# Kernel optimization log

Hardware: AMD Instinct MI355X
Metric: run time of the kernel (lower is better)

The kernel has to match this reference:

```python
import jax, jax.numpy as jnp
import numpy as np
from jax import lax

B, T, V, E, H, M = 512, 60, 50000, 300, 512, 256


def _lstm_final_h(x_emb, seqlen, kernel, bias):
    """BasicLSTMCell (gate order i,j,f,o; forget_bias=1.0) with dynamic_rnn
    sequence_length semantics: state stops updating at t >= seqlen.
    x_emb: [B, T, E]; returns final h: [B, H]."""
    b = x_emb.shape[0]
    h0 = jnp.zeros((b, H), x_emb.dtype)
    c0 = jnp.zeros((b, H), x_emb.dtype)

    def step(carry, inp):
        c, h = carry
        xt, t = inp
        z = jnp.concatenate([xt, h], axis=1) @ kernel + bias  # [B, 4H]
        i, j, f, o = jnp.split(z, 4, axis=1)
        nc = c * jax.nn.sigmoid(f + 1.0) + jax.nn.sigmoid(i) * jnp.tanh(j)
        nh = jnp.tanh(nc) * jax.nn.sigmoid(o)
        valid = (t < seqlen)[:, None]
        return (jnp.where(valid, nc, c), jnp.where(valid, nh, h)), None

    (c, h), _ = lax.scan(step, (c0, h0),
                         (jnp.swapaxes(x_emb, 0, 1), jnp.arange(T)))
    return h


def setup_inputs() -> dict:
    key = jax.random.key(0)
    ks = jax.random.split(key, 8)
    return {
        "input1": jax.random.randint(ks[0], (B, T), 0, V, dtype=jnp.int32),
        "input2": jax.random.randint(ks[1], (B, T), 0, V, dtype=jnp.int32),
        "seqlen1": jax.random.randint(ks[2], (B,), 1, T + 1, dtype=jnp.int32),
        "seqlen2": jax.random.randint(ks[3], (B,), 1, T + 1, dtype=jnp.int32),
        "embeddings": jax.random.normal(ks[4], (V, E), jnp.float32) * 0.1,
        "lstm_kernel": jax.random.normal(ks[5], (E + H, 4 * H), jnp.float32) * 0.02,
        "lstm_bias": jnp.zeros((4 * H,), jnp.float32),
        "W1": jax.random.normal(ks[6], (4 * (H + 1) + 1, M), jnp.float32) * 0.02,
        "b1": jnp.zeros((1, M), jnp.float32),
        "W2": jax.random.normal(ks[7], (M, 2), jnp.float32) * 0.02,
        "b2": jnp.zeros((1, 2), jnp.float32),
    }


def reference(input1, input2, seqlen1, seqlen2, embeddings,
              lstm_kernel, lstm_bias, W1, b1, W2, b2):
    x1 = embeddings[input1]  # [B, T, E]
    x2 = embeddings[input2]
    h1 = _lstm_final_h(x1, seqlen1, lstm_kernel, lstm_bias)  # [B, H]
    h2 = _lstm_final_h(x2, seqlen2, lstm_kernel, lstm_bias)
    len1 = (seqlen1.astype(jnp.float32) / float(T))[:, None]
    len2 = (seqlen2.astype(jnp.float32) / float(T))[:, None]
    h1 = jnp.concatenate([h1, len1], axis=1)  # [B, H+1]
    h2 = jnp.concatenate([h2, len2], axis=1)
    h_sub = h1 - h2
    h_dist = jnp.sum(h_sub * h_sub, axis=1, keepdims=True)  # [B, 1]
    h_mul = h1 * h2
    h_combined = jnp.concatenate([h1, h2, h_sub, h_dist, h_mul], axis=1)
    e1 = jax.nn.relu(h_combined @ W1 + b1)  # dropout keep_prob=1 -> identity
    preds = e1 @ W2 + b2  # [B, 2]
    return preds
```

## Files before the change

kernel.cpp:

```cpp
#include <hip/hip_runtime.h>
#include <hip/hip_bf16.h>

#define BATCH 512
#define TT 60
#define EDIM 300
#define HDIM 512
#define KREAL 812
#define KP 896
#define KP1 2112
#define MDIM 256

typedef __bf16 bf16x4 __attribute__((ext_vector_type(4)));
typedef __bf16 bf16x8 __attribute__((ext_vector_type(8)));
typedef float  f32x16 __attribute__((ext_vector_type(16)));

#define GLL16(g, l) __builtin_amdgcn_global_load_lds( \
    (const __attribute__((address_space(1))) void*)(g), \
    (__attribute__((address_space(3))) void*)(l), 16, 0, 0)

__device__ __forceinline__ float sigm(float x) {
    return 1.0f / (1.0f + __expf(-x));
}
__device__ __forceinline__ float tanh_fast(float x) {
    float e = __expf(-2.0f * fabsf(x));
    float r = (1.0f - e) / (1.0f + e);
    return x >= 0.0f ? r : -r;
}


__global__ __launch_bounds__(256) void sort_rows(const int* __restrict__ sl1,
                                                 const int* __restrict__ sl2,
                                                 int* __restrict__ rowinfo,
                                                 unsigned* __restrict__ nact) {
    __shared__ unsigned cnt[61];
    __shared__ unsigned off[61];
    int tid = threadIdx.x;
    if (tid < 61) cnt[tid] = 0;
    __syncthreads();
    for (int i = tid; i < 1024; i += 256) {
        int sl = (i < 512) ? sl1[i] : sl2[i - 512];
        atomicAdd(&cnt[60 - sl], 1u);
    }
    __syncthreads();
    if (tid == 0) {
        unsigned s = 0;
        for (int k = 0; k < 61; ++k) { off[k] = s; s += cnt[k]; }
        for (int t = 0; t < 60; ++t) {
            unsigned act = off[60 - t];
            nact[t] = (act + 63) >> 6;
        }
    }
    __syncthreads();
    for (int i = tid; i < 1024; i += 256) {
        int sc = i >= 512;
        int b = i & 511;
        int sl = sc ? sl2[b] : sl1[b];
        unsigned pos = atomicAdd(&off[60 - sl], 1u);
        rowinfo[pos] = b | (sc << 15) | (sl << 20);
    }
}

__global__ __launch_bounds__(256) void prep_w(const float* __restrict__ kern,
                                              __bf16* __restrict__ wf) {
    __shared__ float tile[64][65];
    int bk = blockIdx.x % 14;
    int bn = blockIdx.x / 14;
    int k0 = bk * 64, n0 = bn * 64;
    int tid = threadIdx.x;
#pragma unroll
    for (int i = 0; i < 16; ++i) {
        int id = i * 256 + tid;
        int kk = id >> 6, nn = id & 63;
        int kg = k0 + kk;
        int src = (kg < 300) ? kg : (kg >= 384 ? kg - 84 : -1);
        tile[kk][nn] = (src >= 0) ? kern[(size_t)src * 2048 + n0 + nn] : 0.0f;
    }
    __syncthreads();
    int gate = n0 >> 9;
    int nt = gate >> 1;
#pragma unroll
    for (int i = 0; i < 2; ++i) {
        int id = i * 256 + tid;
        int nn = id >> 3, k8 = id & 7;
        bf16x8 hv, lv;
#pragma unroll
        for (int j = 0; j < 8; ++j) {
            float v = tile[k8 * 8 + j][nn];
            __bf16 h = (__bf16)v;
            hv[j] = h;
            lv[j] = (__bf16)(v - (float)h);
        }
        int cg = (((n0 & 511) >> 4) + (nn >> 4));
        int hc = nn & 15;
        int lzc = ((gate & 1) << 4) + hc;
        int kglob = k0 + k8 * 8;
        int c = kglob >> 7;
        int j = (kglob >> 4) & 7;
        int half = k8 & 1;
        size_t o = (size_t)cg * 114688 + c * 16384 + (j * 4 + nt * 2) * 512
                 + (half * 32 + lzc) * 8;
        *(bf16x8*)(wf + o) = hv;
        *(bf16x8*)(wf + o + 512) = lv;
    }
}

__global__ __launch_bounds__(256) void prep_w1(const float* __restrict__ W1,
                                               __bf16* __restrict__ w1h,
                                               __bf16* __restrict__ w1l) {
    __shared__ float tile[64][65];
    int bk = blockIdx.x % 33;
    int bn = blockIdx.x / 33;
    int k0 = bk * 64, n0 = bn * 64;
    int tid = threadIdx.x;
#pragma unroll
    for (int i = 0; i < 16; ++i) {
        int id = i * 256 + tid;
        int kk = id >> 6, nn = id & 63;
        int kg = k0 + kk;
        tile[kk][nn] = (kg < 2053) ? W1[(size_t)kg * MDIM + n0 + nn] : 0.0f;
    }
    __syncthreads();
#pragma unroll
    for (int i = 0; i < 2; ++i) {
        int id = i * 256 + tid;
        int nn = id >> 3, k8 = (id & 7) * 8;
        bf16x8 hv, lv;
#pragma unroll
        for (int j = 0; j < 8; ++j) {
            float v = tile[k8 + j][nn];
            __bf16 h = (__bf16)v;
            hv[j] = h;
            lv[j] = (__bf16)(v - (float)h);
        }
        size_t o = (size_t)(n0 + nn) * KP1 + k0 + k8;
        *(bf16x8*)(w1h + o) = hv;
        *(bf16x8*)(w1l + o) = lv;
    }
}

__device__ __forceinline__ void emb_unit(int tok, int rl, int rr, int bt,
                                         const float* __restrict__ emb,
                                         __bf16* Xfn) {
    const float* er = emb + (size_t)tok * EDIM + rr * 8;
    float4 f0 = *(const float4*)er;
    float4 f1 = (rr == 37) ? make_float4(0.f, 0.f, 0.f, 0.f)
                           : *(const float4*)(er + 4);
    float vv[8] = {f0.x, f0.y, f0.z, f0.w, f1.x, f1.y, f1.z, f1.w};
    bf16x8 hv, lv;
#pragma unroll
    for (int j = 0; j < 8; ++j) {
        __bf16 h = (__bf16)vv[j];
        hv[j] = h;
        lv[j] = (__bf16)(vv[j] - (float)h);
    }
    int ke = rr * 8;
    int c = ke >> 7, kl = ke & 127;
    int kg = kl >> 6, jj = (kl >> 4) & 3, half = (kl >> 3) & 1;
    int s = rl >> 5;
    size_t base = ((((size_t)bt * 2 + s) * 2 + kg) * 7 + c) * 4096 + jj * 1024
                + (half * 32 + (rl & 31)) * 8;
    *(bf16x8*)(Xfn + base) = hv;
    *(bf16x8*)(Xfn + base + 512) = lv;
}

__global__ __launch_bounds__(256) void prep_x0(const int* __restrict__ in1,
                                               const int* __restrict__ in2,
                                               const int* __restrict__ rowinfo,
                                               const float* __restrict__ emb,
                                               __bf16* __restrict__ Xf) {
    __shared__ int tk[64];
    int bt = blockIdx.x >> 5, cg = blockIdx.x & 31;
    int tid = threadIdx.x;
    if (tid < 64) {
        int info = rowinfo[bt * 64 + tid];
        int b = info & 511, sc = (info >> 15) & 1;
        tk[tid] = (sc ? in2 : in1)[b * TT];
    }
    __syncthreads();
    if (tid < 76) {
        int id = tid * 32 + cg;
        int rl = id / 38, rr = id - rl * 38;
        emb_unit(tk[rl], rl, rr, bt, emb, Xf);
    }
}

#define ZSTR 72

__global__ __launch_bounds__(256, 2) void lstm_step(
    int t,
    const int* __restrict__ in1, const int* __restrict__ in2,
    const int* __restrict__ rowinfo, const unsigned* __restrict__ nact,
    const float* __restrict__ emb, const float* __restrict__ bias,
    const __bf16* __restrict__ wf,
    const __bf16* __restrict__ Xf, __bf16* __restrict__ Xfn,
    float* __restrict__ h_state, float* __restrict__ c_state) {

    int bx = blockIdx.x;
    int bt = bx >> 5;
    int cg = ((bx & 7) << 2) | ((bx >> 3) & 3);
    if (bt >= (int)nact[t]) return;

    __shared__ __align__(16) __bf16 Bb[2][16384];
    __shared__ int info_s[64];
    __shared__ int tk[64];

    int tid = threadIdx.x;
    int w = tid >> 6, lane = tid & 63, l31 = lane & 31;
    int s = w >> 1, kg = w & 1;

    if (tid < 64) {
        int info = rowinfo[bt * 64 + tid];
        info_s[tid] = info;
        int b = info & 511, sc = (info >> 15) & 1;
        int tn = (t + 1 < TT) ? t + 1 : t;
        tk[tid] = (sc ? in2 : in1)[b * TT + tn];
    }

    const __bf16* wb = wf + (size_t)cg * 114688;
    auto stageB = [&](int c, int buf) {
        const __bf16* src = wb + c * 16384 + w * 4096 + lane * 8;
        __bf16* dst = &Bb[buf][w * 4096 + lane * 8];
#pragma unroll
        for (int i = 0; i < 8; ++i)
            GLL16(src + i * 512, dst + i * 512);
    };

    const __bf16* Abase = Xf + ((((size_t)bt * 2 + s) * 2 + kg) * 7) * 4096
                        + lane * 8;

    f32x16 acc[2];
#pragma unroll
    for (int nt = 0; nt < 2; ++nt)
#pragma unroll
        for (int r = 0; r < 16; ++r) acc[nt][r] = 0.0f;

    bf16x8 aH[4], aL[4];
    stageB(0, 0);
#pragma unroll
    for (int jj = 0; jj < 4; ++jj) {
        aH[jj] = *(const bf16x8*)(Abase + jj * 1024);
        aL[jj] = *(const bf16x8*)(Abase + jj * 1024 + 512);
    }
    __syncthreads();

#pragma unroll
    for (int c = 0; c < 7; ++c) {
        int cur = c & 1;
        bf16x8 nH[4], nL[4];
        if (c < 6) {
            stageB(c + 1, 1 - cur);
            const __bf16* An = Abase + (c + 1) * 4096;
#pragma unroll
            for (int jj = 0; jj < 4; ++jj) {
                nH[jj] = *(const bf16x8*)(An + jj * 1024);
                nL[jj] = *(const bf16x8*)(An + jj * 1024 + 512);
            }
        }
#pragma unroll
        for (int jj = 0; jj < 4; ++jj) {
            int j = kg * 4 + jj;
#pragma unroll
            for (int nt = 0; nt < 2; ++nt) {
                int T0 = (j * 4 + nt * 2) * 512 + lane * 8;
                bf16x8 bh = *(const bf16x8*)(&Bb[cur][T0]);
                bf16x8 bl = *(const bf16x8*)(&Bb[cur][T0 + 512]);
                acc[nt] = __builtin_amdgcn_mfma_f32_32x32x16_bf16(aH[jj], bh, acc[nt], 0, 0, 0);
                acc[nt] = __builtin_amdgcn_mfma_f32_32x32x16_bf16(aH[jj], bl, acc[nt], 0, 0, 0);
                acc[nt] = __builtin_amdgcn_mfma_f32_32x32x16_bf16(aL[jj], bh, acc[nt], 0, 0, 0);
            }
        }
        if (c < 6) {
#pragma unroll
            for (int jj = 0; jj < 4; ++jj) { aH[jj] = nH[jj]; aL[jj] = nL[jj]; }
        }
        __syncthreads();
    }

    float* zs = (float*)&Bb[1][0];
    if (kg == 0) {
#pragma unroll
        for (int nt = 0; nt < 2; ++nt)
#pragma unroll
            for (int r = 0; r < 16; ++r) {
                int rl = s * 32 + (r & 3) + ((r >> 2) << 3) + ((lane >> 5) << 2);
                zs[rl * ZSTR + nt * 32 + l31] = acc[nt][r];
            }
    }
    __syncthreads();
    if (kg == 1) {
#pragma unroll
        for (int nt = 0; nt < 2; ++nt)
#pragma unroll
            for (int r = 0; r < 16; ++r) {
                int rl = s * 32 + (r & 3) + ((r >> 2) << 3) + ((lane >> 5) << 2);
                zs[rl * ZSTR + nt * 32 + l31] += acc[nt][r];
            }
    }
    __syncthreads();

    __bf16* zh = &Bb[0][0];
    int hc16 = tid & 15;
    int hcol = (cg << 4) + hc16;
    float bi = bias[hcol], bj = bias[512 + hcol];
    float bfv = bias[1024 + hcol], bo = bias[1536 + hcol];
#pragma unroll
    for (int i = 0; i < 4; ++i) {
        int rl = i * 16 + (tid >> 4);
        int info = info_s[rl];
        int b = info & 511, sc = (info >> 15) & 1, sl = info >> 20;
        float zi = zs[rl * ZSTR + hc16]      + bi;
        float zj = zs[rl * ZSTR + 16 + hc16] + bj;
        float zf = zs[rl * ZSTR + 32 + hc16] + bfv;
        float zo = zs[rl * ZSTR + 48 + hc16] + bo;
        size_t co = (size_t)(bt * 64 + rl) * HDIM + hcol;
        size_t ho = (size_t)((sc << 9) + b) * HDIM + hcol;
        float c_old = c_state[co];
        float h_old = h_state[ho];
        float nc = c_old * sigm(zf + 1.0f) + sigm(zi) * tanh_fast(zj);
        float nh = tanh_fast(nc) * sigm(zo);
        bool valid = t < sl;
        float cs = valid ? nc : c_old;
        float hs = valid ? nh : h_old;
        c_state[co] = cs;
        h_state[ho] = hs;
        __bf16 hh = (__bf16)hs;
        int grp = hc16 >> 3, e = hc16 & 7;
        zh[(grp * 64 + rl) * 8 + e] = hh;
        zh[((2 + grp) * 64 + rl) * 8 + e] = (__bf16)(hs - (float)hh);
    }
    __syncthreads();

    if (t + 1 < TT) {
        int plane = tid >> 7;
        int grp = (tid >> 6) & 1;
        int rl = tid & 63;
        bf16x8 val = *(const bf16x8*)(zh + ((plane * 2 + grp) * 64 + rl) * 8);
        int s2 = rl >> 5;
        int c2 = 3 + (cg >> 3);
        int kg2 = (cg >> 2) & 1;
        int jj2 = cg & 3;
        size_t base = ((((size_t)bt * 2 + s2) * 2 + kg2) * 7 + c2) * 4096
                    + jj2 * 1024 + plane * 512 + (grp * 32 + (rl & 31)) * 8;
        *(bf16x8*)(Xfn + base) = val;
        if (tid < 76) {
            int id = tid * 32 + cg;
            int rl2 = id / 38, rr = id - rl2 * 38;
            emb_unit(tk[rl2], rl2, rr, bt, emb, Xfn);
        }
    }
}

__global__ __launch_bounds__(256) void head1(const float* __restrict__ h_state,
                                             const int* __restrict__ sl1,
                                             const int* __restrict__ sl2,
                                             __bf16* __restrict__ hch,
                                             __bf16* __restrict__ hcl) {
    int b = blockIdx.x;
    int tid = threadIdx.x;
    const float* h1 = h_state + (size_t)b * HDIM;
    const float* h2 = h_state + (size_t)(512 + b) * HDIM;
    size_t ro = (size_t)b * KP1;
    float l1 = (float)sl1[b] / (float)TT;
    float l2 = (float)sl2[b] / (float)TT;
    float part = 0.0f;
#pragma unroll
    for (int i = 0; i < 2; ++i) {
        int k = i * 256 + tid;
        float a = h1[k], c = h2[k];
        float sv = a - c;
        float mv = a * c;
        __bf16 xh;
        xh = (__bf16)a;  hch[ro + k] = xh;         hcl[ro + k] = (__bf16)(a - (float)xh);
        xh = (__bf16)c;  hch[ro + 513 + k] = xh;   hcl[ro + 513 + k] = (__bf16)(c - (float)xh);
        xh = (__bf16)sv; hch[ro + 1026 + k] = xh;  hcl[ro + 1026 + k] = (__bf16)(sv - (float)xh);
        xh = (__bf16)mv; hch[ro + 1540 + k] = xh;  hcl[ro + 1540 + k] = (__bf16)(mv - (float)xh);
        part += sv * sv;
    }
    __shared__ float red[4];
#pragma unroll
    for (int off = 32; off > 0; off >>= 1) part += __shfl_down(part, off, 64);
    if ((tid & 63) == 0) red[tid >> 6] = part;
    __syncthreads();
    if (tid == 0) {
        float d = red[0] + red[1] + red[2] + red[3];
        float ls = l1 - l2;
        d += ls * ls;
        float vals[5] = {l1, l2, ls, d, l1 * l2};
        int pos[5] = {512, 1025, 1538, 1539, 2052};
#pragma unroll
        for (int i = 0; i < 5; ++i) {
            __bf16 xh = (__bf16)vals[i];
            hch[ro + pos[i]] = xh;
            hcl[ro + pos[i]] = (__bf16)(vals[i] - (float)xh);
        }
    }
}

__global__ __launch_bounds__(512, 2) void head2m(
    const __bf16* __restrict__ hch, const __bf16* __restrict__ hcl,
    const __bf16* __restrict__ w1h, const __bf16* __restrict__ w1l,
    float* __restrict__ part) {

    __shared__ __align__(16) __bf16 Bb[2][64 * 512];

    int tid = threadIdx.x;
    int bx = blockIdx.x;
    int mt = bx >> 3;
    int n2 = (bx >> 2) & 1;
    int ks = bx & 3;
    int w = tid >> 6, lane = tid & 63, l31 = lane & 31;
    int half8 = (lane >> 5) << 3;
    int s = w >> 1, nh = w & 1;
    int kbase = ks * 528;

    int k8 = tid & 15;
    int jb = k8 >> 1;
    int rb = (tid >> 4) & 31;
    size_t gboff[8];
    int lo[8];
#pragma unroll
    for (int i = 0; i < 8; ++i) {
        int r = ((i & 3) << 5) + rb;
        int plane = i >> 2;
        int ng = n2 * 128 + r;
        gboff[i] = (size_t)ng * KP1 + k8 * 8;
        int nt = r >> 5;
        int colp = ((r & 31) + (jb << 2)) & 31;
        lo[i] = ((((jb << 2) + nt) << 1) + plane) * 512 + (colp + ((k8 & 1) << 5)) * 8;
    }

    const __bf16* Ah0 = hch + (size_t)(mt * 128 + s * 32 + l31) * KP1 + kbase + half8;
    const __bf16* Al0 = hcl + (size_t)(mt * 128 + s * 32 + l31) * KP1 + kbase + half8;

    bf16x8 rB[8];
    f32x16 acc[2];
#pragma unroll
    for (int nt = 0; nt < 2; ++nt)
#pragma unroll
        for (int r = 0; r < 16; ++r) acc[nt][r] = 0.0f;

#pragma unroll
    for (int i = 0; i < 8; ++i)
        rB[i] = *(const bf16x8*)(((i >= 4) ? w1l : w1h) + gboff[i] + kbase);
#pragma unroll
    for (int i = 0; i < 8; ++i) *(bf16x8*)(&Bb[0][lo[i]]) = rB[i];
    __syncthreads();

    for (int c = 0; c < 5; ++c) {
        int cur = c & 1;
        if (c < 4) {
            int k0 = kbase + (c + 1) * 128;
            bool tail = (c + 1 == 4);
#pragma unroll
            for (int i = 0; i < 8; ++i) {
                if (!tail || k8 < 2)
                    rB[i] = *(const bf16x8*)(((i >= 4) ? w1l : w1h) + gboff[i] + k0);
            }
        }
        int jmax = (c == 4) ? 1 : 8;
        for (int j = 0; j < jmax; ++j) {
            bf16x8 ah = *(const bf16x8*)(Ah0 + c * 128 + j * 16);
            bf16x8 al = *(const bf16x8*)(Al0 + c * 128 + j * 16);
            int cp = ((l31 + (j << 2)) & 31) + ((lane >> 5) << 5);
#pragma unroll
            for (int ntl = 0; ntl < 2; ++ntl) {
                int ntg = nh * 2 + ntl;
                const __bf16* bp = &Bb[cur][(((j << 2) + ntg) << 1) * 512 + cp * 8];
                bf16x8 bh = *(const bf16x8*)bp;
                bf16x8 bl = *(const bf16x8*)(bp + 512);
                acc[ntl] = __builtin_amdgcn_mfma_f32_32x32x16_bf16(ah, bh, acc[ntl], 0, 0, 0);
                acc[ntl] = __builtin_amdgcn_mfma_f32_32x32x16_bf16(ah, bl, acc[ntl], 0, 0, 0);
                acc[ntl] = __builtin_amdgcn_mfma_f32_32x32x16_bf16(al, bh, acc[ntl], 0, 0, 0);
            }
        }
        if (c < 4) {
#pragma unroll
            for (int i = 0; i < 8; ++i) *(bf16x8*)(&Bb[1 - cur][lo[i]]) = rB[i];
        }
        __syncthreads();
    }

#pragma unroll
    for (int ntl = 0; ntl < 2; ++ntl)
#pragma unroll
        for (int r = 0; r < 16; ++r) {
            int row = mt * 128 + s * 32 + (r & 3) + ((r >> 2) << 3) + ((lane >> 5) << 2);
            int col = n2 * 128 + nh * 64 + ntl * 32 + l31;
            part[((size_t)ks * 512 + row) * MDIM + col] = acc[ntl][r];
        }
}

__global__ __launch_bounds__(256) void head3(const float* __restrict__ part,
                                             const float* __restrict__ b1,
                                             const float* __restrict__ W2,
                                             const float* __restrict__ b2,
                                             float* __restrict__ out) {
    int row = blockIdx.x;
    int tid = threadIdx.x;
    float sv = b1[tid];
#pragma unroll
    for (int ks = 0; ks < 4; ++ks)
        sv += part[((size_t)ks * 512 + row) * MDIM + tid];
    float e = fmaxf(sv, 0.0f);
    float p0 = e * W2[tid * 2 + 0];
    float p1 = e * W2[tid * 2 + 1];
#pragma unroll
    for (int off = 32; off > 0; off >>= 1) {
        p0 += __shfl_down(p0, off, 64);
        p1 += __shfl_down(p1, off, 64);
    }
    __shared__ float r0[4], r1[4];
    if ((tid & 63) == 0) { r0[tid >> 6] = p0; r1[tid >> 6] = p1; }
    __syncthreads();
    if (tid == 0) out[row * 2 + 0] = r0[0] + r0[1] + r0[2] + r0[3] + b2[0];
    if (tid == 1) out[row * 2 + 1] = r1[0] + r1[1] + r1[2] + r1[3] + b2[1];
}

extern "C" void kernel_launch(void* const* d_in, const int* in_sizes, int n_in,
                              void* d_out, int out_size, void* d_ws, size_t ws_size,
                              hipStream_t stream) {
    const int*   in1  = (const int*)d_in[0];
    const int*   in2  = (const int*)d_in[1];
    const int*   sl1  = (const int*)d_in[2];
    const int*   sl2  = (const int*)d_in[3];
    const float* emb  = (const float*)d_in[4];
    const float* kern = (const float*)d_in[5];
    const float* bias = (const float*)d_in[6];
    const float* W1   = (const float*)d_in[7];
    const float* b1   = (const float*)d_in[8];
    const float* W2   = (const float*)d_in[9];
    const float* b2   = (const float*)d_in[10];
    float* out = (float*)d_out;

    char* ws = (char*)d_ws;
    int*      rowinfo = (int*)ws;
    unsigned* nact    = (unsigned*)(ws + 4096u);
    float*  h_state = (float*)(ws + 2097152u);
    float*  c_state = (float*)(ws + 4194304u);
    __bf16* Xf0 = (__bf16*)(ws + 6291456u);
    __bf16* Xf1 = (__bf16*)(ws + 9961472u);
    __bf16* wf  = (__bf16*)(ws + 13631488u);
    __bf16* hch = (__bf16*)(ws + 20971520u);
    __bf16* hcl = (__bf16*)(ws + 23134208u);
    __bf16* w1h = (__bf16*)(ws + 25296896u);
    __bf16* w1l = (__bf16*)(ws + 26378240u);
    float*  part = (float*)(ws + 27459584u);

    hipMemsetAsync(ws + 2097152u, 0, 7864320u, stream);
    hipMemsetAsync(ws + 20971520u, 0, 4325376u, stream);

    sort_rows<<<dim3(1), dim3(256), 0, stream>>>(sl1, sl2, rowinfo, nact);
    prep_w<<<dim3(14 * 32), dim3(256), 0, stream>>>(kern, wf);
    prep_w1<<<dim3(33 * 4), dim3(256), 0, stream>>>(W1, w1h, w1l);
    prep_x0<<<dim3(512), dim3(256), 0, stream>>>(in1, in2, rowinfo, emb, Xf0);

    for (int t = 0; t < TT; ++t) {
        __bf16* Xf  = (t & 1) ? Xf1 : Xf0;
        __bf16* Xfn = (t & 1) ? Xf0 : Xf1;
        lstm_step<<<dim3(512), dim3(256), 0, stream>>>(
            t, in1, in2, rowinfo, nact, emb, bias, wf, Xf, Xfn,
            h_state, c_state);
    }

    head1<<<dim3(512), dim3(256), 0, stream>>>(h_state, sl1, sl2, hch, hcl);
    head2m<<<dim3(32), dim3(512), 0, stream>>>(hch, hcl, w1h, w1l, part);
    head3<<<dim3(512), dim3(256), 0, stream>>>(part, b1, W2, b2, out);
}
```

Baseline: 1.091 ms.

## Load LSTM weights directly to registers with 4-way split-K reduction in LDS

Drops the LDS double-buffered weight staging via global_load_lds and its per-chunk barriers. Each wave now loads both A and B fragments straight from global memory into registers, prefetching one chunk ahead, and covers both row halves over a quarter of the K range. The four partial sums are written to separate LDS slices, with padded stride 66, and summed in the gate epilogue. This removes the in-loop syncs, at the cost of more register pressure and more global traffic for weights, since they are no longer shared through LDS.

```diff
diff --git a/kernel.cpp b/kernel.cpp
--- a/kernel.cpp
+++ b/kernel.cpp
@@ -13,10 +13,6 @@
 typedef __bf16 bf16x4 __attribute__((ext_vector_type(4)));
 typedef __bf16 bf16x8 __attribute__((ext_vector_type(8)));
 typedef float  f32x16 __attribute__((ext_vector_type(16)));
-
-#define GLL16(g, l) __builtin_amdgcn_global_load_lds( \
-    (const __attribute__((address_space(1))) void*)(g), \
-    (__attribute__((address_space(3))) void*)(l), 16, 0, 0)
 
 __device__ __forceinline__ float sigm(float x) {
     return 1.0f / (1.0f + __expf(-x));
@@ -184,7 +180,7 @@
     }
 }
 
-#define ZSTR 72
+#define ZSTR 66
 
 __global__ __launch_bounds__(256, 2) void lstm_step(
     int t,
@@ -200,13 +196,14 @@
     int cg = ((bx & 7) << 2) | ((bx >> 3) & 3);
     if (bt >= (int)nact[t]) return;
 
-    __shared__ __align__(16) __bf16 Bb[2][16384];
+    __shared__ float zs[4 * 64 * ZSTR];
+    __shared__ __bf16 zh[4 * 64 * 8];
     __shared__ int info_s[64];
     __shared__ int tk[64];
 
     int tid = threadIdx.x;
     int w = tid >> 6, lane = tid & 63, l31 = lane & 31;
-    int s = w >> 1, kg = w & 1;
+    int kg = w & 1, jjh = w >> 1;
 
     if (tid < 64) {
         int info = rowinfo[bt * 64 + tid];
@@ -216,89 +213,104 @@
         tk[tid] = (sc ? in2 : in1)[b * TT + tn];
     }
 
-    const __bf16* wb = wf + (size_t)cg * 114688;
-    auto stageB = [&](int c, int buf) {
-        const __bf16* src = wb + c * 16384 + w * 4096 + lane * 8;
-        __bf16* dst = &Bb[buf][w * 4096 + lane * 8];
-#pragma unroll
-        for (int i = 0; i < 8; ++i)
-            GLL16(src + i * 512, dst + i * 512);
-    };
-
-    const __bf16* Abase = Xf + ((((size_t)bt * 2 + s) * 2 + kg) * 7) * 4096
-                        + lane * 8;
-
-    f32x16 acc[2];
-#pragma unroll
-    for (int nt = 0; nt < 2; ++nt)
-#pragma unroll
-        for (int r = 0; r < 16; ++r) acc[nt][r] = 0.0f;
-
-    bf16x8 aH[4], aL[4];
-    stageB(0, 0);
-#pragma unroll
-    for (int jj = 0; jj < 4; ++jj) {
-        aH[jj] = *(const bf16x8*)(Abase + jj * 1024);
-        aL[jj] = *(const bf16x8*)(Abase + jj * 1024 + 512);
-    }
-    __syncthreads();
+    const __bf16* Ab = Xf + (size_t)bt * 114688 + (size_t)kg * 28672
+                     + (size_t)jjh * 2048 + lane * 8;
+    const __bf16* Bbp = wf + (size_t)cg * 114688 + ((kg * 4 + jjh * 2) * 4) * 512
+                      + lane * 8;
+
+    f32x16 acc[2][2];
+#pragma unroll
+    for (int s = 0; s < 2; ++s)
+#pragma unroll
+        for (int nt = 0; nt < 2; ++nt)
+#pragma unroll
+            for (int r = 0; r < 16; ++r) acc[s][nt][r] = 0.0f;
+
+    bf16x8 cAh[2][2], cAl[2][2], cBh[2][2], cBl[2][2];
+    bf16x8 nAh[2][2], nAl[2][2], nBh[2][2], nBl[2][2];
+
+#pragma unroll
+    for (int s = 0; s < 2; ++s)
+#pragma unroll
+        for (int j2 = 0; j2 < 2; ++j2) {
+            const __bf16* ap = Ab + s * 57344 + j2 * 1024;
+            cAh[s][j2] = *(const bf16x8*)ap;
+            cAl[s][j2] = *(const bf16x8*)(ap + 512);
+        }
+#pragma unroll
+    for (int j2 = 0; j2 < 2; ++j2)
+#pragma unroll
+        for (int nt = 0; nt < 2; ++nt) {
+            const __bf16* bp = Bbp + (j2 * 4 + nt * 2) * 512;
+            cBh[j2][nt] = *(const bf16x8*)bp;
+            cBl[j2][nt] = *(const bf16x8*)(bp + 512);
+        }
 
 #pragma unroll
     for (int c = 0; c < 7; ++c) {
-        int cur = c & 1;
-        bf16x8 nH[4], nL[4];
         if (c < 6) {
-            stageB(c + 1, 1 - cur);
-            const __bf16* An = Abase + (c + 1) * 4096;
-#pragma unroll
-            for (int jj = 0; jj < 4; ++jj) {
-                nH[jj] = *(const bf16x8*)(An + jj * 1024);
-                nL[jj] = *(const bf16x8*)(An + jj * 1024 + 512);
-            }
-        }
-#pragma unroll
-        for (int jj = 0; jj < 4; ++jj) {
-            int j = kg * 4 + jj;
-#pragma unroll
-            for (int nt = 0; nt < 2; ++nt) {
-                int T0 = (j * 4 + nt * 2) * 512 + lane * 8;
-                bf16x8 bh = *(const bf16x8*)(&Bb[cur][T0]);
-                bf16x8 bl = *(const bf16x8*)(&Bb[cur][T0 + 512]);
-                acc[nt] = __builtin_amdgcn_mfma_f32_32x32x16_bf16(aH[jj], bh, acc[nt], 0, 0, 0);
-                acc[nt] = __builtin_amdgcn_mfma_f32_32x32x16_bf16(aH[jj], bl, acc[nt], 0, 0, 0);
-                acc[nt] = __builtin_amdgcn_mfma_f32_32x32x16_bf16(aL[jj], bh, acc[nt], 0, 0, 0);
-            }
-        }
+            const __bf16* An = Ab + (c + 1) * 4096;
+            const __bf16* Bn = Bbp + (c + 1) * 16384;
+#pragma unroll
+            for (int s = 0; s < 2; ++s)
+#pragma unroll
+                for (int j2 = 0; j2 < 2; ++j2) {
+                    const __bf16* ap = An + s * 57344 + j2 * 1024;
+                    nAh[s][j2] = *(const bf16x8*)ap;
+                    nAl[s][j2] = *(const bf16x8*)(ap + 512);
+                }
+#pragma unroll
+            for (int j2 = 0; j2 < 2; ++j2)
+#pragma unroll
+                for (int nt = 0; nt < 2; ++nt) {
+                    const __bf16* bp = Bn + (j2 * 4 + nt * 2) * 512;
+                    nBh[j2][nt] = *(const bf16x8*)bp;
+                    nBl[j2][nt] = *(const bf16x8*)(bp + 512);
+                }
+        }
+#pragma unroll
+        for (int j2 = 0; j2 < 2; ++j2)
+#pragma unroll
+            for (int s = 0; s < 2; ++s)
+#pragma unroll
+                for (int nt = 0; nt < 2; ++nt) {
+                    acc[s][nt] = __builtin_amdgcn_mfma_f32_32x32x16_bf16(
+                        cAh[s][j2], cBh[j2][nt], acc[s][nt], 0, 0, 0);
+                    acc[s][nt] = __builtin_amdgcn_mfma_f32_32x32x16_bf16(
+                        cAh[s][j2], cBl[j2][nt], acc[s][nt], 0, 0, 0);
+                    acc[s][nt] = __builtin_amdgcn_mfma_f32_32x32x16_bf16(
+                        cAl[s][j2], cBh[j2][nt], acc[s][nt], 0, 0, 0);
+                }
         if (c < 6) {
 #pragma unroll
-            for (int jj = 0; jj < 4; ++jj) { aH[jj] = nH[jj]; aL[jj] = nL[jj]; }
-        }
-        __syncthreads();
-    }
-
-    float* zs = (float*)&Bb[1][0];
-    if (kg == 0) {
+            for (int s = 0; s < 2; ++s)
+#pragma unroll
+                for (int j2 = 0; j2 < 2; ++j2) {
+                    cAh[s][j2] = nAh[s][j2];
+                    cAl[s][j2] = nAl[s][j2];
+                }
+#pragma unroll
+            for (int j2 = 0; j2 < 2; ++j2)
+#pragma unroll
+                for (int nt = 0; nt < 2; ++nt) {
+                    cBh[j2][nt] = nBh[j2][nt];
+                    cBl[j2][nt] = nBl[j2][nt];
+                }
+        }
+    }
+
+    float* zw = zs + w * (64 * ZSTR);
+#pragma unroll
+    for (int s = 0; s < 2; ++s)
 #pragma unroll
         for (int nt = 0; nt < 2; ++nt)
 #pragma unroll
             for (int r = 0; r < 16; ++r) {
                 int rl = s * 32 + (r & 3) + ((r >> 2) << 3) + ((lane >> 5) << 2);
-                zs[rl * ZSTR + nt * 32 + l31] = acc[nt][r];
+                zw[rl * ZSTR + nt * 32 + l31] = acc[s][nt][r];
             }
-    }
-    __syncthreads();
-    if (kg == 1) {
-#pragma unroll
-        for (int nt = 0; nt < 2; ++nt)
-#pragma unroll
-            for (int r = 0; r < 16; ++r) {
-                int rl = s * 32 + (r & 3) + ((r >> 2) << 3) + ((lane >> 5) << 2);
-                zs[rl * ZSTR + nt * 32 + l31] += acc[nt][r];
-            }
-    }
-    __syncthreads();
-
-    __bf16* zh = &Bb[0][0];
+    __syncthreads();
+
     int hc16 = tid & 15;
     int hcol = (cg << 4) + hc16;
     float bi = bias[hcol], bj = bias[512 + hcol];
@@ -308,10 +320,16 @@
         int rl = i * 16 + (tid >> 4);
         int info = info_s[rl];
         int b = info & 511, sc = (info >> 15) & 1, sl = info >> 20;
-        float zi = zs[rl * ZSTR + hc16]      + bi;
-        float zj = zs[rl * ZSTR + 16 + hc16] + bj;
-        float zf = zs[rl * ZSTR + 32 + hc16] + bfv;
-        float zo = zs[rl * ZSTR + 48 + hc16] + bo;
+        float zi = 0.f, zj = 0.f, zf = 0.f, zo = 0.f;
+#pragma unroll
+        for (int q = 0; q < 4; ++q) {
+            const float* zp = zs + q * (64 * ZSTR) + rl * ZSTR;
+            zi += zp[hc16];
+            zj += zp[16 + hc16];
+            zf += zp[32 + hc16];
+            zo += zp[48 + hc16];
+        }
+        zi += bi; zj += bj; zf += bfv; zo += bo;
         size_t co = (size_t)(bt * 64 + rl) * HDIM + hcol;
         size_t ho = (size_t)((sc << 9) + b) * HDIM + hcol;
         float c_old = c_state[co];
```

Result: slower. 1.129 ms (+3.5%).
